# Kernel optimization log

Measured on AMD Instinct MI355X. Metric: run time of the kernel, lower is better.

The kernel has to match this reference:

```python
import jax, jax.numpy as jnp
import numpy as np
from jax import lax

KERNEL = 3
ALPHA = 0.85
C1 = 0.01 ** 2
C2 = 0.03 ** 2


def _avg_pool(x, k):
    # stride-1 VALID average pool over the last two (H, W) dims of NCHW input
    s = lax.reduce_window(x, 0.0, lax.add, (1, 1, k, k), (1, 1, 1, 1), 'VALID')
    return s / (k * k)


def setup_inputs() -> dict:
    key = jax.random.key(0)
    k1, k2 = jax.random.split(key)
    shape = (4, 3, 1080, 1920)
    pred = jax.random.uniform(k1, shape, dtype=jnp.float32)
    gt = jax.random.uniform(k2, shape, dtype=jnp.float32)
    return {"pred": pred, "gt": gt}


def reference(pred, gt):
    p = (KERNEL - 1) // 2
    # reflection pad H and W
    x = jnp.pad(pred, ((0, 0), (0, 0), (p, p), (p, p)), mode='reflect')
    y = jnp.pad(gt, ((0, 0), (0, 0), (p, p), (p, p)), mode='reflect')

    mu_x = _avg_pool(x, KERNEL)
    mu_y = _avg_pool(y, KERNEL)
    sigma_x = _avg_pool(x * x, KERNEL) - mu_x * mu_x
    sigma_y = _avg_pool(y * y, KERNEL) - mu_y * mu_y
    sigma_xy = _avg_pool(x * y, KERNEL) - mu_x * mu_y

    ssim_n = (2.0 * mu_x * mu_y + C1) * (2.0 * sigma_xy + C2)
    ssim_d = (mu_x * mu_x + mu_y * mu_y + C1) * (sigma_x + sigma_y + C2)
    ssim_pp = jnp.clip((1.0 - ssim_n / ssim_d) * 0.5, 0.0, 1.0)

    ssim_loss = jnp.mean(ssim_pp, axis=1, keepdims=True)   # [B,1,H,W]
    l1_loss = jnp.mean(jnp.abs(pred - gt), axis=1, keepdims=True)
    return ALPHA * ssim_loss + (1.0 - ALPHA) * l1_loss
```

## Files before the change

### kernel.cpp

```cpp
#include <hip/hip_runtime.h>

#define IMG_H 1080
#define IMG_W 1920
#define CH 3

typedef float f32x2 __attribute__((ext_vector_type(2)));

#if __has_builtin(__builtin_elementwise_fma)
#define FMA2(a, b, c) __builtin_elementwise_fma((a), (b), (c))
#else
#define FMA2(a, b, c) ((a) * (b) + (c))
#endif

__device__ __forceinline__ float dpp_up1(float x) {
    int i = __float_as_int(x);
    return __int_as_float(__builtin_amdgcn_update_dpp(i, i, 0x138, 0xF, 0xF, false));
}
__device__ __forceinline__ float dpp_dn1(float x) {
    int i = __float_as_int(x);
    return __int_as_float(__builtin_amdgcn_update_dpp(i, i, 0x130, 0xF, 0xF, false));
}

__global__ __launch_bounds__(256)
void dssim_l1_kernel(const float* __restrict__ pred,
                     const float* __restrict__ gt,
                     float* __restrict__ out) {
    constexpr float K1 = 81.0f * 0.0001f;
    constexpr float K2 = 81.0f * 0.0009f;

    const f32x2 k1_ = K1, k2_ = K2;
    const f32x2 two_ = 2.0f, m2_ = -2.0f, e18_ = 18.0f, n9_ = 9.0f;
    const f32x2 mh_ = -0.5f, h_ = 0.5f, zero_ = 0.0f, one_ = 1.0f;
    const f32x2 a3_ = 0.85f / 3.0f, b3_ = 0.15f / 3.0f;

    const int lane = threadIdx.x;
    const int r0   = (blockIdx.y * 4 + threadIdx.y) * 2;
    const int b    = blockIdx.z;
    const int c0   = blockIdx.x * 128 + 2 * lane;

    const int rws[4] = { (r0 == 0) ? 1 : r0 - 1,
                         r0, r0 + 1,
                         (r0 + 2 == IMG_H) ? IMG_H - 2 : r0 + 2 };

    const bool l0 = (lane == 0), l63 = (lane == 63);
    const bool limg = l0  && (blockIdx.x == 0);
    const bool rimg = l63 && (blockIdx.x == 14);
    const int  hcol = l0 ? max(c0 - 1, 0) : min(c0 + 2, IMG_W - 1);
    const bool is_edge = l0 || l63;

    const size_t img = (size_t)IMG_H * IMG_W;
    const float* __restrict__ pb[2 * CH] = {
        pred + (size_t)b * CH * img,
        pred + (size_t)b * CH * img + img,
        pred + (size_t)b * CH * img + 2 * img,
        gt   + (size_t)b * CH * img,
        gt   + (size_t)b * CH * img + img,
        gt   + (size_t)b * CH * img + 2 * img };

    unsigned off[4];
#pragma unroll
    for (int i = 0; i < 4; ++i) off[i] = (unsigned)rws[i] * IMG_W + (unsigned)c0;

    float hx[4][CH], hy[4][CH];
    if (is_edge) {
        const unsigned hbase = (unsigned)hcol - (unsigned)c0;
#pragma unroll
        for (int i = 0; i < 4; ++i) {
            const unsigned ho = off[i] + hbase;
#pragma unroll
            for (int c = 0; c < CH; ++c) {
                hx[i][c] = pb[c][ho];
                hy[i][c] = pb[CH + c][ho];
            }
        }
    }

    f32x2 qx[4][CH], qy[4][CH];
#pragma unroll
    for (int i = 0; i < 4; ++i) {
#pragma unroll
        for (int c = 0; c < CH; ++c) {
            qx[i][c] = *reinterpret_cast<const f32x2*>(pb[c]      + off[i]);
            qy[i][c] = *reinterpret_cast<const f32x2*>(pb[CH + c] + off[i]);
        }
    }

    f32x2 Ax[CH], Ay[CH], Aw[CH], Ap[CH];
    f32x2 Bx[CH], By[CH], Bw[CH], Bp[CH];

#define CONSUME(I, DOA, FIRSTA, DOB, FIRSTB)                                \
    _Pragma("unroll")                                                       \
    for (int c = 0; c < CH; ++c) {                                          \
        const f32x2 qxv = qx[I][c], qyv = qy[I][c];                         \
        float xm = dpp_up1(qxv.y), ym = dpp_up1(qyv.y);                     \
        float xp = dpp_dn1(qxv.x), yp = dpp_dn1(qyv.x);                     \
        if (l0)   { xm = hx[I][c]; ym = hy[I][c]; }                         \
        if (l63)  { xp = hx[I][c]; yp = hy[I][c]; }                         \
        if (limg) { xm = qxv.y; ym = qyv.y; }            \
        if (rimg) { xp = qxv.x; yp = qyv.x; }       \
        const f32x2 X0 = { xm, qxv.x }, X2 = { qxv.y, xp };                 \
        const f32x2 Y0 = { ym, qyv.x }, Y2 = { qyv.y, yp };                 \
        const f32x2 WX = X0 + qxv + X2;                                     \
        const f32x2 WY = Y0 + qyv + Y2;                                     \
        const f32x2 WP = FMA2(X2, Y2, FMA2(qxv, qyv, X0 * Y0));             \
        const f32x2 WW = FMA2(X2, X2, FMA2(Y2, Y2, FMA2(qxv, qxv,           \
                         FMA2(qyv, qyv, FMA2(X0, X0, Y0 * Y0)))));          \
        if (DOA) {                                                          \
            if (FIRSTA) { Ax[c] = WX; Ay[c] = WY; Aw[c] = WW; Ap[c] = WP; } \
            else        { Ax[c] += WX; Ay[c] += WY;                         \
                          Aw[c] += WW; Ap[c] += WP; }                       \
        }                                                                   \
        if (DOB) {                                                          \
            if (FIRSTB) { Bx[c] = WX; By[c] = WY; Bw[c] = WW; Bp[c] = WP; } \
            else        { Bx[c] += WX; By[c] += WY;                         \
                          Bw[c] += WW; Bp[c] += WP; }                       \
        }                                                                   \
    }

    CONSUME(0, true, true,  false, false)
    CONSUME(1, true, false, true,  true)
    CONSUME(2, true, false, true,  false)
    CONSUME(3, false, false, true, false)
#undef CONSUME

    f32x2 l1r0 = zero_, l1r1 = zero_;
#pragma unroll
    for (int c = 0; c < CH; ++c) {
#if __has_builtin(__builtin_elementwise_abs)
        l1r0 += __builtin_elementwise_abs(qx[1][c] - qy[1][c]);
        l1r1 += __builtin_elementwise_abs(qx[2][c] - qy[2][c]);
#else
        f32x2 d0 = qx[1][c] - qy[1][c], d1 = qx[2][c] - qy[2][c];
        d0.x = fabsf(d0.x); d0.y = fabsf(d0.y);
        d1.x = fabsf(d1.x); d1.y = fabsf(d1.y);
        l1r0 += d0; l1r1 += d1;
#endif
    }

#define SSIM2(AX, AY, AW, AP, ACC)                                          \
    {                                                                       \
        const f32x2 u  = (AX) * (AY);                                       \
        const f32x2 v  = FMA2((AY), (AY), (AX) * (AX));                     \
        const f32x2 n1 = FMA2(two_, u, k1_);                                \
        const f32x2 n2 = FMA2(e18_, (AP), FMA2(m2_, u, k2_));               \
        const f32x2 d1 = v + k1_;                                           \
        const f32x2 d2 = FMA2(n9_, (AW), k2_) - v;                          \
        const f32x2 nd = n1 * n2, dd = d1 * d2;                             \
        f32x2 rc;                                                           \
        rc.x = __builtin_amdgcn_rcpf(dd.x);                                 \
        rc.y = __builtin_amdgcn_rcpf(dd.y);                                 \
        f32x2 s = FMA2(mh_, nd * rc, h_);                                   \
        s = __builtin_elementwise_min(                                      \
                __builtin_elementwise_max(s, zero_), one_);                 \
        ACC = FMA2(a3_, s, ACC);                                            \
    }

    f32x2 o0 = b3_ * l1r0;
    f32x2 o1 = b3_ * l1r1;
#pragma unroll
    for (int c = 0; c < CH; ++c) {
        SSIM2(Ax[c], Ay[c], Aw[c], Ap[c], o0)
        SSIM2(Bx[c], By[c], Bw[c], Bp[c], o1)
    }
#undef SSIM2

    float* op = out + ((size_t)b * IMG_H + r0) * IMG_W + c0;
    __builtin_nontemporal_store(o0, reinterpret_cast<f32x2*>(op));
    __builtin_nontemporal_store(o1, reinterpret_cast<f32x2*>(op + IMG_W));
}

extern "C" void kernel_launch(void* const* d_in, const int* in_sizes, int n_in,
                              void* d_out, int out_size, void* d_ws, size_t ws_size,
                              hipStream_t stream) {
    const float* pred = (const float*)d_in[0];
    const float* gt   = (const float*)d_in[1];
    float* out = (float*)d_out;

    dim3 block(64, 4, 1);
    dim3 grid(IMG_W / 128, IMG_H / 8, 4);
    dssim_l1_kernel<<<grid, block, 0, stream>>>(pred, gt, out);
}
```

Before: 57.51 us.

## Process two independent row-pair streams per thread with half-size blocks

Each thread now computes two separate 2-row output strips (rows r and r+4) instead of one, with all 48 vector loads for both strips issued up front to raise memory-level parallelism per thread. The block shrinks to 64x2 threads so the grid shape stays the same. Row reflection moves into a helper, and the output stores change from nontemporal to regular stores. This trades occupancy and register pressure for more outstanding loads per wave, and the store change may affect cache behavior.

```diff
diff --git a/kernel.cpp b/kernel.cpp
--- a/kernel.cpp
+++ b/kernel.cpp
@@ -21,7 +21,11 @@
     return __int_as_float(__builtin_amdgcn_update_dpp(i, i, 0x130, 0xF, 0xF, false));
 }
 
-__global__ __launch_bounds__(256)
+__device__ __forceinline__ int reflect_row(int r) {
+    return (r < 0) ? -r : ((r >= IMG_H) ? 2 * IMG_H - 2 - r : r);
+}
+
+__global__ __launch_bounds__(128)
 void dssim_l1_kernel(const float* __restrict__ pred,
                      const float* __restrict__ gt,
                      float* __restrict__ out) {
@@ -33,19 +37,19 @@
     const f32x2 mh_ = -0.5f, h_ = 0.5f, zero_ = 0.0f, one_ = 1.0f;
     const f32x2 a3_ = 0.85f / 3.0f, b3_ = 0.15f / 3.0f;
 
-    const int lane = threadIdx.x;
-    const int r0   = (blockIdx.y * 4 + threadIdx.y) * 2;
-    const int b    = blockIdx.z;
-    const int c0   = blockIdx.x * 128 + 2 * lane;
-
-    const int rws[4] = { (r0 == 0) ? 1 : r0 - 1,
-                         r0, r0 + 1,
-                         (r0 + 2 == IMG_H) ? IMG_H - 2 : r0 + 2 };
+    const int lane  = threadIdx.x;
+    const int ty    = threadIdx.y;
+    const int b     = blockIdx.z;
+    const int c0    = blockIdx.x * 128 + 2 * lane;
+    const int rbase = blockIdx.y * 8 + ty * 2;
+    const int r0a   = rbase;
+    const int r0b   = rbase + 4;
 
     const bool l0 = (lane == 0), l63 = (lane == 63);
     const bool limg = l0  && (blockIdx.x == 0);
     const bool rimg = l63 && (blockIdx.x == 14);
     const int  hcol = l0 ? max(c0 - 1, 0) : min(c0 + 2, IMG_W - 1);
+    const unsigned hbase = (unsigned)(hcol - c0);
     const bool is_edge = l0 || l63;
 
     const size_t img = (size_t)IMG_H * IMG_W;
@@ -57,45 +61,63 @@
         gt   + (size_t)b * CH * img + img,
         gt   + (size_t)b * CH * img + 2 * img };
 
-    unsigned off[4];
-#pragma unroll
-    for (int i = 0; i < 4; ++i) off[i] = (unsigned)rws[i] * IMG_W + (unsigned)c0;
-
-    float hx[4][CH], hy[4][CH];
+    unsigned off_a[4], off_b[4];
+    {
+        const int ra0 = reflect_row(r0a - 1);
+        const int ra3 = reflect_row(r0a + 2);
+        const int rb3 = reflect_row(r0b + 2);
+        off_a[0] = (unsigned)ra0 * IMG_W + (unsigned)c0;
+        off_a[1] = (unsigned)r0a * IMG_W + (unsigned)c0;
+        off_a[2] = (unsigned)(r0a + 1) * IMG_W + (unsigned)c0;
+        off_a[3] = (unsigned)ra3 * IMG_W + (unsigned)c0;
+        off_b[0] = (unsigned)(r0b - 1) * IMG_W + (unsigned)c0;
+        off_b[1] = (unsigned)r0b * IMG_W + (unsigned)c0;
+        off_b[2] = (unsigned)(r0b + 1) * IMG_W + (unsigned)c0;
+        off_b[3] = (unsigned)rb3 * IMG_W + (unsigned)c0;
+    }
+
+    float hx_a[4][CH], hy_a[4][CH], hx_b[4][CH], hy_b[4][CH];
     if (is_edge) {
-        const unsigned hbase = (unsigned)hcol - (unsigned)c0;
 #pragma unroll
         for (int i = 0; i < 4; ++i) {
-            const unsigned ho = off[i] + hbase;
+            const unsigned ha = off_a[i] + hbase;
+            const unsigned hb = off_b[i] + hbase;
 #pragma unroll
             for (int c = 0; c < CH; ++c) {
-                hx[i][c] = pb[c][ho];
-                hy[i][c] = pb[CH + c][ho];
+                hx_a[i][c] = pb[c][ha];
+                hy_a[i][c] = pb[CH + c][ha];
+                hx_b[i][c] = pb[c][hb];
+                hy_b[i][c] = pb[CH + c][hb];
             }
         }
     }
 
-    f32x2 qx[4][CH], qy[4][CH];
+    f32x2 qx_a[4][CH], qy_a[4][CH], qx_b[4][CH], qy_b[4][CH];
 #pragma unroll
     for (int i = 0; i < 4; ++i) {
 #pragma unroll
         for (int c = 0; c < CH; ++c) {
-            qx[i][c] = *reinterpret_cast<const f32x2*>(pb[c]      + off[i]);
-            qy[i][c] = *reinterpret_cast<const f32x2*>(pb[CH + c] + off[i]);
+            qx_a[i][c] = *reinterpret_cast<const f32x2*>(pb[c]      + off_a[i]);
+            qy_a[i][c] = *reinterpret_cast<const f32x2*>(pb[CH + c] + off_a[i]);
         }
     }
-
-    f32x2 Ax[CH], Ay[CH], Aw[CH], Ap[CH];
-    f32x2 Bx[CH], By[CH], Bw[CH], Bp[CH];
-
-#define CONSUME(I, DOA, FIRSTA, DOB, FIRSTB)                                \
+#pragma unroll
+    for (int i = 0; i < 4; ++i) {
+#pragma unroll
+        for (int c = 0; c < CH; ++c) {
+            qx_b[i][c] = *reinterpret_cast<const f32x2*>(pb[c]      + off_b[i]);
+            qy_b[i][c] = *reinterpret_cast<const f32x2*>(pb[CH + c] + off_b[i]);
+        }
+    }
+
+#define CONSUME(S, I, DOA, FIRSTA, DOB, FIRSTB)                             \
     _Pragma("unroll")                                                       \
     for (int c = 0; c < CH; ++c) {                                          \
-        const f32x2 qxv = qx[I][c], qyv = qy[I][c];                         \
+        const f32x2 qxv = qx_##S[I][c], qyv = qy_##S[I][c];                 \
         float xm = dpp_up1(qxv.y), ym = dpp_up1(qyv.y);                     \
         float xp = dpp_dn1(qxv.x), yp = dpp_dn1(qyv.x);                     \
-        if (l0)   { xm = hx[I][c]; ym = hy[I][c]; }                         \
-        if (l63)  { xp = hx[I][c]; yp = hy[I][c]; }                         \
+        if (l0)   { xm = hx_##S[I][c]; ym = hy_##S[I][c]; }                 \
+        if (l63)  { xp = hx_##S[I][c]; yp = hy_##S[I][c]; }                 \
         if (limg) { xm = qxv.y; ym = qyv.y; }            \
         if (rimg) { xp = qxv.x; yp = qyv.x; }       \
         const f32x2 X0 = { xm, qxv.x }, X2 = { qxv.y, xp };                 \
@@ -115,26 +137,6 @@
             else        { Bx[c] += WX; By[c] += WY;                         \
                           Bw[c] += WW; Bp[c] += WP; }                       \
         }                                                                   \
-    }
-
-    CONSUME(0, true, true,  false, false)
-    CONSUME(1, true, false, true,  true)
-    CONSUME(2, true, false, true,  false)
-    CONSUME(3, false, false, true, false)
-#undef CONSUME
-
-    f32x2 l1r0 = zero_, l1r1 = zero_;
-#pragma unroll
-    for (int c = 0; c < CH; ++c) {
-#if __has_builtin(__builtin_elementwise_abs)
-        l1r0 += __builtin_elementwise_abs(qx[1][c] - qy[1][c]);
-        l1r1 += __builtin_elementwise_abs(qx[2][c] - qy[2][c]);
-#else
-        f32x2 d0 = qx[1][c] - qy[1][c], d1 = qx[2][c] - qy[2][c];
-        d0.x = fabsf(d0.x); d0.y = fabsf(d0.y);
-        d1.x = fabsf(d1.x); d1.y = fabsf(d1.y);
-        l1r0 += d0; l1r1 += d1;
-#endif
     }
 
 #define SSIM2(AX, AY, AW, AP, ACC)                                          \
@@ -155,18 +157,41 @@
         ACC = FMA2(a3_, s, ACC);                                            \
     }
 
-    f32x2 o0 = b3_ * l1r0;
-    f32x2 o1 = b3_ * l1r1;
-#pragma unroll
-    for (int c = 0; c < CH; ++c) {
-        SSIM2(Ax[c], Ay[c], Aw[c], Ap[c], o0)
-        SSIM2(Bx[c], By[c], Bw[c], Bp[c], o1)
-    }
+#define STREAM_BODY(S, R0)                                                  \
+    {                                                                       \
+        f32x2 Ax[CH], Ay[CH], Aw[CH], Ap[CH];                               \
+        f32x2 Bx[CH], By[CH], Bw[CH], Bp[CH];                               \
+        CONSUME(S, 0, true, true,  false, false)                            \
+        CONSUME(S, 1, true, false, true,  true)                             \
+        CONSUME(S, 2, true, false, true,  false)                            \
+        CONSUME(S, 3, false, false, true, false)                            \
+        f32x2 l1r0 = zero_, l1r1 = zero_;                                   \
+        _Pragma("unroll")                                                   \
+        for (int c = 0; c < CH; ++c) {                                      \
+            f32x2 d0 = qx_##S[1][c] - qy_##S[1][c];                         \
+            f32x2 d1 = qx_##S[2][c] - qy_##S[2][c];                         \
+            d0.x = fabsf(d0.x); d0.y = fabsf(d0.y);                         \
+            d1.x = fabsf(d1.x); d1.y = fabsf(d1.y);                         \
+            l1r0 += d0; l1r1 += d1;                                         \
+        }                                                                   \
+        f32x2 o0 = b3_ * l1r0;                                              \
+        f32x2 o1 = b3_ * l1r1;                                              \
+        _Pragma("unroll")                                                   \
+        for (int c = 0; c < CH; ++c) {                                      \
+            SSIM2(Ax[c], Ay[c], Aw[c], Ap[c], o0)                           \
+            SSIM2(Bx[c], By[c], Bw[c], Bp[c], o1)                           \
+        }                                                                   \
+        float* op = out + ((size_t)b * IMG_H + (R0)) * IMG_W + c0;          \
+        *reinterpret_cast<f32x2*>(op) = o0;                                 \
+        *reinterpret_cast<f32x2*>(op + IMG_W) = o1;                         \
+    }
+
+    STREAM_BODY(a, r0a)
+    STREAM_BODY(b, r0b)
+
+#undef STREAM_BODY
 #undef SSIM2
-
-    float* op = out + ((size_t)b * IMG_H + r0) * IMG_W + c0;
-    __builtin_nontemporal_store(o0, reinterpret_cast<f32x2*>(op));
-    __builtin_nontemporal_store(o1, reinterpret_cast<f32x2*>(op + IMG_W));
+#undef CONSUME
 }
 
 extern "C" void kernel_launch(void* const* d_in, const int* in_sizes, int n_in,
@@ -176,7 +201,7 @@
     const float* gt   = (const float*)d_in[1];
     float* out = (float*)d_out;
 
-    dim3 block(64, 4, 1);
+    dim3 block(64, 2, 1);
     dim3 grid(IMG_W / 128, IMG_H / 8, 4);
     dssim_l1_kernel<<<grid, block, 0, stream>>>(pred, gt, out);
 }
```

New measurement: 68.24 us. +18.7%, slower.
